# Optimization experiments

Measured on AMD Instinct MI355X. Metric: run time of the kernel, lower is better.

## Reference

```python
import jax, jax.numpy as jnp
import numpy as np

ATOM = 8          # atom_size
STRIDE = 4
NB_ATOMS = 256
LMBDA = 0.1       # l1 prox weight (prox_params)
NONDIFF = 20      # nondiff_steps (run under stop_gradient, mirroring torch.no_grad)
DIFF = 5          # diff_steps


def setup_inputs() -> dict:
    key = jax.random.key(0)
    k1, k2 = jax.random.split(key)
    y = jax.random.normal(k1, (8, 3, 256, 256), dtype=jnp.float32)
    # atoms ~ N(0,1)/sqrt(nb_channels*atom_size^2), as in __init__ with init='random'
    atoms = jax.random.normal(k2, (NB_ATOMS, 3, ATOM, ATOM), dtype=jnp.float32) / np.float32(np.sqrt(3 * ATOM * ATOM))
    return {"y": y, "atoms": atoms}


def _forward(y, atoms):
    B, C, H, W = y.shape
    a, s = ATOM, STRIDE
    Hp = (H - a) // s + 1
    Wp = (W - a) // s + 1
    D = C * a * a

    # patch row/col index grids: rows[ph, i] = ph*s + i
    rows = (jnp.arange(Hp) * s)[:, None] + jnp.arange(a)          # [Hp, a]
    cols = (jnp.arange(Wp) * s)[:, None] + jnp.arange(a)          # [Wp, a]
    R4 = rows[:, :, None, None]                                    # [Hp, a, 1, 1]
    C4 = cols[None, None, :, :]                                    # [1, 1, Wp, a]

    # unfold: extract overlapping patches -> [B, C, Hp, a, Wp, a] -> [N, D] (channel-major, matching torch)
    p6 = y[:, :, R4, C4]
    p = p6.transpose(0, 2, 4, 1, 3, 5).reshape(B * Hp * Wp, D)     # N = B*Hp*Wp

    mean = jnp.mean(p, axis=1, keepdims=True)                      # per-patch mean
    p = p - mean

    # l2-normalize atoms
    A = atoms.reshape(NB_ATOMS, D)
    A = A / jnp.linalg.norm(A, axis=1, keepdims=True)              # [nA, D]

    X = A @ A.T                                                    # [nA, nA] Gram matrix
    q = A @ p.T                                                    # [nA, N]
    L = jnp.linalg.norm(X, 2)                                      # spectral norm (Lipschitz const)
    thr = LMBDA / L

    def ista_step(c, _):
        c = c - (X @ c - q) / L
        c = jnp.sign(c) * jnp.maximum(jnp.abs(c) - thr, 0.0)       # soft-threshold prox
        return c, None

    c0 = jnp.zeros((NB_ATOMS, q.shape[1]), dtype=q.dtype)
    c, _ = jax.lax.scan(ista_step, c0, None, length=NONDIFF)
    c = jax.lax.stop_gradient(c)                                    # torch.no_grad() warmup
    c, _ = jax.lax.scan(ista_step, c, None, length=DIFF)

    # reconstruct patches: einsum('ij,il->jl') = c.T @ A, add mean back
    rec = c.T @ A + mean                                            # [N, D]
    p6r = rec.reshape(B, Hp, Wp, C, a, a).transpose(0, 3, 1, 4, 2, 5)  # [B, C, Hp, a, Wp, a]

    # fold: overlap-add patches back to image
    out = jnp.zeros((B, C, H, W), dtype=y.dtype).at[:, :, R4, C4].add(p6r)
    counts = jnp.zeros((H, W), dtype=y.dtype).at[R4, C4].add(
        jnp.ones((Hp, a, Wp, a), dtype=y.dtype))                    # overlap divisors
    return out / counts


def reference(y, atoms):
    return _forward(y, atoms)
```

## Files before the change

### kernel.cpp

```cpp
#include <hip/hip_runtime.h>
#include <math.h>

#define NPATCH 31752
#define TILE   32
#define PSTR   200
#define CSTR   264
#define MSTR   200

typedef _Float16 f16;
typedef __attribute__((ext_vector_type(2))) _Float16 f16x2;
typedef __attribute__((ext_vector_type(4))) _Float16 f16x4;
typedef __attribute__((ext_vector_type(8))) _Float16 f16x8;
typedef __attribute__((ext_vector_type(2))) __fp16   hf16x2;
typedef __attribute__((ext_vector_type(4))) float    f32x4;
#define MFMA16 __builtin_amdgcn_mfma_f32_16x16x32_f16

union HU { f16x2 h; hf16x2 g; unsigned u; };

__device__ __forceinline__ f16x2 pk2(float a, float b)
{
    HU r; r.g = __builtin_amdgcn_cvt_pkrtz(a, b);
    return r.h;
}

__device__ __forceinline__ f16x2 shrink2(f16x2 v, f16x2 thr2)
{
    HU a; a.h = v;
    unsigned sgn = a.u & 0x80008000u;
    a.u &= 0x7FFF7FFFu;
    f16x2 t = a.h - thr2;
    t = __builtin_elementwise_max(t, (f16x2)(f16)0);
    HU r; r.h = t; r.u |= sgn;
    return r.h;
}

__global__ void norm_kernel(const float* __restrict__ atoms, float* __restrict__ A,
                            float* __restrict__ As)
{
    int b = blockIdx.x, t = threadIdx.x;
    float v0 = atoms[b*192 + t];
    float v1 = atoms[b*192 + t + 64];
    float v2 = atoms[b*192 + t + 128];
    float s  = v0*v0 + v1*v1 + v2*v2;
    float r  = v0 + v1 + v2;
    #pragma unroll
    for (int m = 1; m < 64; m <<= 1) { s += __shfl_xor(s, m, 64); r += __shfl_xor(r, m, 64); }
    float rn = 1.0f / sqrtf(s);
    A[b*192 + t]       = v0 * rn;
    A[b*192 + t + 64]  = v1 * rn;
    A[b*192 + t + 128] = v2 * rn;
    if (t == 0) As[b] = r * rn;
}

__global__ void packab_kernel(const float* __restrict__ A,
                              f16* __restrict__ Ap, f16* __restrict__ Ab)
{
    int e = blockIdx.x * 256 + threadIdx.x;
    if (e < 49152) {
        int j = e & 7, lane = (e >> 3) & 63, t = e >> 9, ks = t % 6, I = t / 6;
        int row = I*16 + (lane & 15), col = ks*32 + (lane >> 4)*8 + j;
        Ap[e] = (f16)A[row*192 + col];
    } else {
        int u = e - 49152;
        int j = u & 7, lane = (u >> 3) & 63, t = u >> 9, ks = t & 7, dt = t >> 3;
        int k = ks*32 + (lane >> 4)*8 + j, d = dt*16 + (lane & 15);
        Ab[u] = (f16)A[k*192 + d];
    }
}

__global__ __launch_bounds__(256, 1)
void lchain_kernel(const f16* __restrict__ Ab, float* __restrict__ scal)
{
    __shared__ f16   mls[2 * 192 * MSTR];
    __shared__ float red[4];
    __shared__ float trc[16];
    const int tid = threadIdx.x, wv = tid >> 6, lane = tid & 63;
    const int quad = lane >> 4, l16 = lane & 15;
    const f16x8* AbV = (const f16x8*)Ab;

    f32x4 acc[3][12];
    #pragma unroll
    for (int it = 0; it < 3; ++it)
        #pragma unroll
        for (int J = 0; J < 12; ++J) acc[it][J] = (f32x4){0,0,0,0};
    for (int ks = 0; ks < 8; ++ks) {
        f16x8 bf[12];
        #pragma unroll
        for (int J = 0; J < 12; ++J) bf[J] = AbV[(J*8 + ks)*64 + lane];
        #pragma unroll
        for (int it = 0; it < 3; ++it) {
            f16x8 af = AbV[((3*wv + it)*8 + ks)*64 + lane];
            #pragma unroll
            for (int J = 0; J < 12; ++J)
                acc[it][J] = MFMA16(af, bf[J], acc[it][J], 0, 0, 0);
        }
    }
    #pragma unroll
    for (int it = 0; it < 3; ++it)
        #pragma unroll
        for (int J = 0; J < 12; ++J)
            #pragma unroll
            for (int g = 0; g < 4; ++g)
                mls[((3*wv + it)*16 + quad*4 + g)*MSTR + J*16 + l16] = (f16)acc[it][J][g];
    __syncthreads();

    float rprev = 1.0f;
    for (int t = 1; t <= 8; ++t) {
        const f16* src = mls + ((t & 1) ^ 1) * (192 * MSTR);
        f16*       dst = mls + (t & 1) * (192 * MSTR);
        const float inv = 1.0f / rprev;

        f32x4 a2[3][12];
        #pragma unroll
        for (int it = 0; it < 3; ++it)
            #pragma unroll
            for (int J = 0; J < 12; ++J) a2[it][J] = (f32x4){0,0,0,0};
        for (int ks = 0; ks < 6; ++ks) {
            f16x8 bf[12];
            #pragma unroll
            for (int J = 0; J < 12; ++J)
                bf[J] = *(const f16x8*)&src[(J*16 + l16)*MSTR + ks*32 + quad*8];
            #pragma unroll
            for (int it = 0; it < 3; ++it) {
                f16x8 af = *(const f16x8*)&src[((3*wv + it)*16 + l16)*MSTR + ks*32 + quad*8];
                #pragma unroll
                for (int J = 0; J < 12; ++J)
                    a2[it][J] = MFMA16(af, bf[J], a2[it][J], 0, 0, 0);
            }
        }
        float dsum = 0.0f;
        #pragma unroll
        for (int it = 0; it < 3; ++it) {
            int I = 3*wv + it;
            #pragma unroll
            for (int J = 0; J < 12; ++J)
                #pragma unroll
                for (int g = 0; g < 4; ++g) {
                    float v = a2[it][J][g] * inv * inv;
                    dst[(I*16 + quad*4 + g)*MSTR + J*16 + l16] = (f16)v;
                    if (J == I && l16 == quad*4 + g) dsum += v;
                }
        }
        #pragma unroll
        for (int m = 1; m < 64; m <<= 1) dsum += __shfl_xor(dsum, m, 64);
        if (lane == 0) red[wv] = dsum;
        __syncthreads();
        float r = red[0] + red[1] + red[2] + red[3];
        if (tid == 0) trc[t] = r;
        rprev = r;
        __syncthreads();
    }
    if (tid == 0) {
        float a = 0.0f;
        #pragma unroll
        for (int u = 1; u <= 8; ++u) a += exp2f(-(float)u) * log2f(trc[u]);
        float L = exp2f(a);
        scal[16] = 1.0f / L;
        scal[17] = 0.1f / L;
    }
}

__global__ void gpack_kernel(const float* __restrict__ A, const float* __restrict__ scal,
                             f16* __restrict__ Gp)
{
    __shared__ float arow[192];
    __shared__ float xrow[256];
    int i = blockIdx.x, j = threadIdx.x;
    const float invL = scal[16];
    if (j < 192) arow[j] = A[i*192 + j];
    __syncthreads();
    float s = 0.0f;
    #pragma unroll 4
    for (int d = 0; d < 192; d += 4) {
        float4 av = *(const float4*)&A[j*192 + d];
        s += arow[d]*av.x + arow[d+1]*av.y + arow[d+2]*av.z + arow[d+3]*av.w;
    }
    xrow[j] = (i == j ? 1.0f : 0.0f) - s * invL;
    __syncthreads();
    if (j < 32) {
        int ks = j >> 2, q = j & 3;
        f16x8 h;
        #pragma unroll
        for (int u = 0; u < 8; ++u) h[u] = (f16)xrow[ks*32 + q*8 + u];
        int I = i >> 4, lane = q*16 + (i & 15);
        *(f16x8*)&Gp[(((I*8 + ks)*64) + lane)*8] = h;
    }
}

__global__ __launch_bounds__(256, 2)
void mega_kernel(const float* __restrict__ y,
                 const f16* __restrict__ Gp, const f16* __restrict__ Ap,
                 const f16* __restrict__ Ab, const float* __restrict__ As,
                 const float* __restrict__ scal, float* __restrict__ out)
{
    __shared__ f16      p_lds[TILE * PSTR];
    __shared__ f16      c_lds[TILE * CSTR];
    __shared__ float    mean_lds[TILE];
    __shared__ float    msum[256];
    __shared__ unsigned pco[TILE];

    const int tid  = threadIdx.x;
    const int base = blockIdx.x * TILE;
    const int wv = tid >> 6, lane = tid & 63, quad = lane >> 4, l16 = lane & 15;
    const float invL = scal[16];
    const float thr  = scal[17];
    const f16x2 thr2 = { (f16)thr, (f16)thr };

    f16x8 greg[4][8];
    {
        const f16x8* GpV = (const f16x8*)Gp;
        #pragma unroll
        for (int rt = 0; rt < 4; ++rt)
            #pragma unroll
            for (int ks = 0; ks < 8; ++ks)
                greg[rt][ks] = GpV[((wv*4 + rt)*8 + ks)*64 + lane];
    }

    {
        int n_l = tid >> 3, qq = tid & 7;
        int n = base + n_l; if (n >= NPATCH) n = NPATCH - 1;
        int b = n / 3969, rem = n - b * 3969;
        int r = rem / 63, sc = rem - r * 63;
        if (qq == 0) pco[n_l] = ((unsigned)b << 16) | ((unsigned)r << 8) | (unsigned)sc;
        float s = 0.0f;
        #pragma unroll
        for (int u = 0; u < 3; ++u) {
            int d  = qq * 24 + u * 8;
            int ch = d >> 6, id = (d & 63) >> 3;
            const float* src = &y[((b*3 + ch)*256 + (r*4 + id))*256 + sc*4];
            float4 a = *(const float4*)src;
            float4 bq = *(const float4*)(src + 4);
            s += a.x + a.y + a.z + a.w + bq.x + bq.y + bq.z + bq.w;
            f16x8 h = { (f16)a.x, (f16)a.y, (f16)a.z, (f16)a.w,
                        (f16)bq.x, (f16)bq.y, (f16)bq.z, (f16)bq.w };
            *(f16x8*)&p_lds[n_l * PSTR + d] = h;
        }
        msum[tid] = s;
    }
    __syncthreads();
    if (tid < TILE) {
        float s = 0.0f;
        #pragma unroll
        for (int u = 0; u < 8; ++u) s += msum[tid*8 + u];
        mean_lds[tid] = s * (1.0f / 192.0f);
    }
    __syncthreads();

    f32x4 qf[4][2];
    #pragma unroll
    for (int rt = 0; rt < 4; ++rt)
        #pragma unroll
        for (int ct = 0; ct < 2; ++ct) qf[rt][ct] = (f32x4){0,0,0,0};

    const f16x8* ApV = (const f16x8*)Ap;
    #pragma unroll
    for (int ks = 0; ks < 6; ++ks) {
        f16x8 bf[2];
        #pragma unroll
        for (int ct = 0; ct < 2; ++ct)
            bf[ct] = *(const f16x8*)&p_lds[(ct*16 + l16)*PSTR + ks*32 + quad*8];
        #pragma unroll
        for (int rt = 0; rt < 4; ++rt) {
            f16x8 af = ApV[((wv*4 + rt)*6 + ks)*64 + lane];
            #pragma unroll
            for (int ct = 0; ct < 2; ++ct)
                qf[rt][ct] = MFMA16(af, bf[ct], qf[rt][ct], 0, 0, 0);
        }
    }

    f16x2 qslo[4][2], qshi[4][2];
    #pragma unroll
    for (int rt = 0; rt < 4; ++rt) {
        float a0 = As[wv*64 + rt*16 + quad*4 + 0];
        float a1 = As[wv*64 + rt*16 + quad*4 + 1];
        float a2 = As[wv*64 + rt*16 + quad*4 + 2];
        float a3 = As[wv*64 + rt*16 + quad*4 + 3];
        #pragma unroll
        for (int ct = 0; ct < 2; ++ct) {
            float mn = mean_lds[ct*16 + l16];
            float q0 = (qf[rt][ct][0] - mn*a0) * invL;
            float q1 = (qf[rt][ct][1] - mn*a1) * invL;
            float q2 = (qf[rt][ct][2] - mn*a2) * invL;
            float q3 = (qf[rt][ct][3] - mn*a3) * invL;
            f16x2 lo = pk2(q0, q1);
            f16x2 hi = pk2(q2, q3);
            qslo[rt][ct] = lo;  qshi[rt][ct] = hi;
            f16x2 clo = shrink2(lo, thr2);
            f16x2 chi = shrink2(hi, thr2);
            f16x4 cc; cc[0]=clo[0]; cc[1]=clo[1]; cc[2]=chi[0]; cc[3]=chi[1];
            *(f16x4*)&c_lds[(ct*16 + l16)*CSTR + wv*64 + rt*16 + quad*4] = cc;
        }
    }
    __syncthreads();

    for (int it = 0; it < 24; ++it) {
        f32x4 af[4][2];
        #pragma unroll
        for (int rt = 0; rt < 4; ++rt)
            #pragma unroll
            for (int ct = 0; ct < 2; ++ct) af[rt][ct] = (f32x4){0,0,0,0};

        #pragma unroll
        for (int ks = 0; ks < 8; ++ks) {
            f16x8 b0 = *(const f16x8*)&c_lds[(l16)*CSTR      + ks*32 + quad*8];
            f16x8 b1 = *(const f16x8*)&c_lds[(16 + l16)*CSTR + ks*32 + quad*8];
            #pragma unroll
            for (int rt = 0; rt < 4; ++rt) {
                af[rt][0] = MFMA16(greg[rt][ks], b0, af[rt][0], 0, 0, 0);
                af[rt][1] = MFMA16(greg[rt][ks], b1, af[rt][1], 0, 0, 0);
            }
        }
        __syncthreads();
        #pragma unroll
        for (int rt = 0; rt < 4; ++rt)
            #pragma unroll
            for (int ct = 0; ct < 2; ++ct) {
                f16x2 vlo = pk2(af[rt][ct][0], af[rt][ct][1]) + qslo[rt][ct];
                f16x2 vhi = pk2(af[rt][ct][2], af[rt][ct][3]) + qshi[rt][ct];
                vlo = shrink2(vlo, thr2);
                vhi = shrink2(vhi, thr2);
                f16x4 cc; cc[0]=vlo[0]; cc[1]=vlo[1]; cc[2]=vhi[0]; cc[3]=vhi[1];
                *(f16x4*)&c_lds[(ct*16 + l16)*CSTR + wv*64 + rt*16 + quad*4] = cc;
            }
        __syncthreads();
    }

    const int nt = wv >> 1, dtb = 6 * (wv & 1);
    f32x4 rf[6];
    #pragma unroll
    for (int u = 0; u < 6; ++u) rf[u] = (f32x4){0,0,0,0};

    const f16x8* AbV = (const f16x8*)Ab;
    #pragma unroll
    for (int ks = 0; ks < 8; ++ks) {
        f16x8 afr = *(const f16x8*)&c_lds[(nt*16 + l16)*CSTR + ks*32 + quad*8];
        #pragma unroll
        for (int u = 0; u < 6; ++u) {
            f16x8 bb = AbV[((dtb + u)*8 + ks)*64 + lane];
            rf[u] = MFMA16(afr, bb, rf[u], 0, 0, 0);
        }
    }
    #pragma unroll
    for (int g = 0; g < 4; ++g) {
        int nl = nt*16 + quad*4 + g;
        int n  = base + nl;
        if (n < NPATCH) {
            unsigned pc = pco[nl];
            int b = pc >> 16, r = (pc >> 8) & 255, sc = pc & 255;
            float mn = mean_lds[nl];
            #pragma unroll
            for (int u = 0; u < 6; ++u) {
                int d  = (dtb + u)*16 + l16;
                int ch = d >> 6, dh = (d & 63) >> 3, dw = d & 7;
                atomicAdd(&out[((b*3 + ch)*256 + (r*4 + dh))*256 + sc*4 + dw],
                          rf[u][g] + mn);
            }
        }
    }
}

__global__ void divcnt_kernel(float* __restrict__ out)
{
    int idx = blockIdx.x * 256 + threadIdx.x;
    int w = idx & 255, h = (idx >> 8) & 255;
    int rlo = max(h - 4, 0) >> 2, rhi = min(62, h >> 2);
    int slo = max(w - 4, 0) >> 2, shi = min(62, w >> 2);
    out[idx] *= 1.0f / (float)((rhi - rlo + 1) * (shi - slo + 1));
}

extern "C" void kernel_launch(void* const* d_in, const int* in_sizes, int n_in,
                              void* d_out, int out_size, void* d_ws, size_t ws_size,
                              hipStream_t stream)
{
    const float* y     = (const float*)d_in[0];
    const float* atoms = (const float*)d_in[1];
    float* out = (float*)d_out;
    float* ws  = (float*)d_ws;

    float* A    = ws;
    float* As   = ws + 49152;
    float* scal = ws + 49408;
    f16*   Ap   = (f16*)(ws + 49440);
    f16*   Ab   = (f16*)(ws + 74016);
    f16*   Gp   = (f16*)(ws + 98592);

    (void)hipMemsetAsync(d_out, 0, (size_t)out_size * sizeof(float), stream);

    norm_kernel  <<<256, 64,  0, stream>>>(atoms, A, As);
    packab_kernel<<<384, 256, 0, stream>>>(A, Ap, Ab);
    lchain_kernel<<<1, 256,   0, stream>>>(Ab, scal);
    gpack_kernel <<<256, 256, 0, stream>>>(A, scal, Gp);
    mega_kernel  <<<(NPATCH + TILE - 1) / TILE, 256, 0, stream>>>
        (y, Gp, Ap, Ab, As, scal, out);
    divcnt_kernel<<<6144, 256, 0, stream>>>(out);
}
```

Baseline: 228.7 us.

## Process two 32-patch subtiles per block with interleaved ISTA and fragment-packed LDS

Doubles the per-block tile to 64 patches, split into two 32-patch subtiles whose ISTA updates are interleaved. Each subtile's Gram-matrix MFMAs run while the other's result is written back, so there is one barrier per subtile half-step instead of a full-tile sync per iteration. The coefficient LDS buffer is rearranged into an MFMA-fragment-packed layout so B operands load as contiguous lane*8 vectors, which removes the padded stride. The cost is twice the q registers, larger LDS, and half as many blocks, which reduces grid parallelism and may lower occupancy.

```diff
diff --git a/kernel.cpp b/kernel.cpp
--- a/kernel.cpp
+++ b/kernel.cpp
@@ -2,9 +2,8 @@
 #include <math.h>
 
 #define NPATCH 31752
-#define TILE   32
+#define TILE   64
 #define PSTR   200
-#define CSTR   264
 #define MSTR   200
 
 typedef _Float16 f16;
@@ -194,9 +193,9 @@
                  const float* __restrict__ scal, float* __restrict__ out)
 {
     __shared__ f16      p_lds[TILE * PSTR];
-    __shared__ f16      c_lds[TILE * CSTR];
+    __shared__ f16      c_lds[2 * 16 * 512];
     __shared__ float    mean_lds[TILE];
-    __shared__ float    msum[256];
+    __shared__ float    msum[512];
     __shared__ unsigned pco[TILE];
 
     const int tid  = threadIdx.x;
@@ -206,6 +205,10 @@
     const float thr  = scal[17];
     const f16x2 thr2 = { (f16)thr, (f16)thr };
 
+    #define CWADDR(st, rt, ct) \
+        ((st)*8192 + ((ct)*8 + (wv*2 + ((rt)>>1)))*512 \
+         + ((((rt)&1)*2 + (quad>>1))*16 + l16)*8 + (quad&1)*4)
+
     f16x8 greg[4][8];
     {
         const f16x8* GpV = (const f16x8*)Gp;
@@ -216,8 +219,9 @@
                 greg[rt][ks] = GpV[((wv*4 + rt)*8 + ks)*64 + lane];
     }
 
-    {
-        int n_l = tid >> 3, qq = tid & 7;
+    #pragma unroll
+    for (int p = 0; p < 2; ++p) {
+        int n_l = p*32 + (tid >> 3), qq = tid & 7;
         int n = base + n_l; if (n >= NPATCH) n = NPATCH - 1;
         int b = n / 3969, rem = n - b * 3969;
         int r = rem / 63, sc = rem - r * 63;
@@ -235,60 +239,62 @@
                         (f16)bq.x, (f16)bq.y, (f16)bq.z, (f16)bq.w };
             *(f16x8*)&p_lds[n_l * PSTR + d] = h;
         }
-        msum[tid] = s;
+        msum[p*256 + tid] = s;
     }
     __syncthreads();
     if (tid < TILE) {
+        int p = tid >> 5, bse = (tid & 31) * 8;
         float s = 0.0f;
         #pragma unroll
-        for (int u = 0; u < 8; ++u) s += msum[tid*8 + u];
+        for (int u = 0; u < 8; ++u) s += msum[p*256 + bse + u];
         mean_lds[tid] = s * (1.0f / 192.0f);
     }
     __syncthreads();
 
-    f32x4 qf[4][2];
-    #pragma unroll
-    for (int rt = 0; rt < 4; ++rt)
-        #pragma unroll
-        for (int ct = 0; ct < 2; ++ct) qf[rt][ct] = (f32x4){0,0,0,0};
-
+    f16x2 qslo[2][4][2], qshi[2][4][2];
     const f16x8* ApV = (const f16x8*)Ap;
     #pragma unroll
-    for (int ks = 0; ks < 6; ++ks) {
-        f16x8 bf[2];
-        #pragma unroll
-        for (int ct = 0; ct < 2; ++ct)
-            bf[ct] = *(const f16x8*)&p_lds[(ct*16 + l16)*PSTR + ks*32 + quad*8];
+    for (int st = 0; st < 2; ++st) {
+        f32x4 qf[4][2];
+        #pragma unroll
+        for (int rt = 0; rt < 4; ++rt)
+            #pragma unroll
+            for (int ct = 0; ct < 2; ++ct) qf[rt][ct] = (f32x4){0,0,0,0};
+        #pragma unroll
+        for (int ks = 0; ks < 6; ++ks) {
+            f16x8 bf[2];
+            #pragma unroll
+            for (int ct = 0; ct < 2; ++ct)
+                bf[ct] = *(const f16x8*)&p_lds[(st*32 + ct*16 + l16)*PSTR + ks*32 + quad*8];
+            #pragma unroll
+            for (int rt = 0; rt < 4; ++rt) {
+                f16x8 af = ApV[((wv*4 + rt)*6 + ks)*64 + lane];
+                #pragma unroll
+                for (int ct = 0; ct < 2; ++ct)
+                    qf[rt][ct] = MFMA16(af, bf[ct], qf[rt][ct], 0, 0, 0);
+            }
+        }
         #pragma unroll
         for (int rt = 0; rt < 4; ++rt) {
-            f16x8 af = ApV[((wv*4 + rt)*6 + ks)*64 + lane];
-            #pragma unroll
-            for (int ct = 0; ct < 2; ++ct)
-                qf[rt][ct] = MFMA16(af, bf[ct], qf[rt][ct], 0, 0, 0);
-        }
-    }
-
-    f16x2 qslo[4][2], qshi[4][2];
-    #pragma unroll
-    for (int rt = 0; rt < 4; ++rt) {
-        float a0 = As[wv*64 + rt*16 + quad*4 + 0];
-        float a1 = As[wv*64 + rt*16 + quad*4 + 1];
-        float a2 = As[wv*64 + rt*16 + quad*4 + 2];
-        float a3 = As[wv*64 + rt*16 + quad*4 + 3];
-        #pragma unroll
-        for (int ct = 0; ct < 2; ++ct) {
-            float mn = mean_lds[ct*16 + l16];
-            float q0 = (qf[rt][ct][0] - mn*a0) * invL;
-            float q1 = (qf[rt][ct][1] - mn*a1) * invL;
-            float q2 = (qf[rt][ct][2] - mn*a2) * invL;
-            float q3 = (qf[rt][ct][3] - mn*a3) * invL;
-            f16x2 lo = pk2(q0, q1);
-            f16x2 hi = pk2(q2, q3);
-            qslo[rt][ct] = lo;  qshi[rt][ct] = hi;
-            f16x2 clo = shrink2(lo, thr2);
-            f16x2 chi = shrink2(hi, thr2);
-            f16x4 cc; cc[0]=clo[0]; cc[1]=clo[1]; cc[2]=chi[0]; cc[3]=chi[1];
-            *(f16x4*)&c_lds[(ct*16 + l16)*CSTR + wv*64 + rt*16 + quad*4] = cc;
+            float a0 = As[wv*64 + rt*16 + quad*4 + 0];
+            float a1 = As[wv*64 + rt*16 + quad*4 + 1];
+            float a2 = As[wv*64 + rt*16 + quad*4 + 2];
+            float a3 = As[wv*64 + rt*16 + quad*4 + 3];
+            #pragma unroll
+            for (int ct = 0; ct < 2; ++ct) {
+                float mn = mean_lds[st*32 + ct*16 + l16];
+                float q0 = (qf[rt][ct][0] - mn*a0) * invL;
+                float q1 = (qf[rt][ct][1] - mn*a1) * invL;
+                float q2 = (qf[rt][ct][2] - mn*a2) * invL;
+                float q3 = (qf[rt][ct][3] - mn*a3) * invL;
+                f16x2 lo = pk2(q0, q1);
+                f16x2 hi = pk2(q2, q3);
+                qslo[st][rt][ct] = lo;  qshi[st][rt][ct] = hi;
+                f16x2 clo = shrink2(lo, thr2);
+                f16x2 chi = shrink2(hi, thr2);
+                f16x4 cc; cc[0]=clo[0]; cc[1]=clo[1]; cc[2]=chi[0]; cc[3]=chi[1];
+                *(f16x4*)&c_lds[CWADDR(st, rt, ct)] = cc;
+            }
         }
     }
     __syncthreads();
@@ -299,11 +305,10 @@
         for (int rt = 0; rt < 4; ++rt)
             #pragma unroll
             for (int ct = 0; ct < 2; ++ct) af[rt][ct] = (f32x4){0,0,0,0};
-
         #pragma unroll
         for (int ks = 0; ks < 8; ++ks) {
-            f16x8 b0 = *(const f16x8*)&c_lds[(l16)*CSTR      + ks*32 + quad*8];
-            f16x8 b1 = *(const f16x8*)&c_lds[(16 + l16)*CSTR + ks*32 + quad*8];
+            f16x8 b0 = *(const f16x8*)&c_lds[(ks)*512 + lane*8];
+            f16x8 b1 = *(const f16x8*)&c_lds[(8 + ks)*512 + lane*8];
             #pragma unroll
             for (int rt = 0; rt < 4; ++rt) {
                 af[rt][0] = MFMA16(greg[rt][ks], b0, af[rt][0], 0, 0, 0);
@@ -315,48 +320,77 @@
         for (int rt = 0; rt < 4; ++rt)
             #pragma unroll
             for (int ct = 0; ct < 2; ++ct) {
-                f16x2 vlo = pk2(af[rt][ct][0], af[rt][ct][1]) + qslo[rt][ct];
-                f16x2 vhi = pk2(af[rt][ct][2], af[rt][ct][3]) + qshi[rt][ct];
+                f16x2 vlo = pk2(af[rt][ct][0], af[rt][ct][1]) + qslo[0][rt][ct];
+                f16x2 vhi = pk2(af[rt][ct][2], af[rt][ct][3]) + qshi[0][rt][ct];
                 vlo = shrink2(vlo, thr2);
                 vhi = shrink2(vhi, thr2);
                 f16x4 cc; cc[0]=vlo[0]; cc[1]=vlo[1]; cc[2]=vhi[0]; cc[3]=vhi[1];
-                *(f16x4*)&c_lds[(ct*16 + l16)*CSTR + wv*64 + rt*16 + quad*4] = cc;
-            }
+                *(f16x4*)&c_lds[CWADDR(0, rt, ct)] = cc;
+            }
+        #pragma unroll
+        for (int rt = 0; rt < 4; ++rt)
+            #pragma unroll
+            for (int ct = 0; ct < 2; ++ct) af[rt][ct] = (f32x4){0,0,0,0};
+        #pragma unroll
+        for (int ks = 0; ks < 8; ++ks) {
+            f16x8 b0 = *(const f16x8*)&c_lds[8192 + (ks)*512 + lane*8];
+            f16x8 b1 = *(const f16x8*)&c_lds[8192 + (8 + ks)*512 + lane*8];
+            #pragma unroll
+            for (int rt = 0; rt < 4; ++rt) {
+                af[rt][0] = MFMA16(greg[rt][ks], b0, af[rt][0], 0, 0, 0);
+                af[rt][1] = MFMA16(greg[rt][ks], b1, af[rt][1], 0, 0, 0);
+            }
+        }
         __syncthreads();
-    }
+        #pragma unroll
+        for (int rt = 0; rt < 4; ++rt)
+            #pragma unroll
+            for (int ct = 0; ct < 2; ++ct) {
+                f16x2 vlo = pk2(af[rt][ct][0], af[rt][ct][1]) + qslo[1][rt][ct];
+                f16x2 vhi = pk2(af[rt][ct][2], af[rt][ct][3]) + qshi[1][rt][ct];
+                vlo = shrink2(vlo, thr2);
+                vhi = shrink2(vhi, thr2);
+                f16x4 cc; cc[0]=vlo[0]; cc[1]=vlo[1]; cc[2]=vhi[0]; cc[3]=vhi[1];
+                *(f16x4*)&c_lds[CWADDR(1, rt, ct)] = cc;
+            }
+    }
+    __syncthreads();
 
     const int nt = wv >> 1, dtb = 6 * (wv & 1);
-    f32x4 rf[6];
-    #pragma unroll
-    for (int u = 0; u < 6; ++u) rf[u] = (f32x4){0,0,0,0};
-
     const f16x8* AbV = (const f16x8*)Ab;
     #pragma unroll
-    for (int ks = 0; ks < 8; ++ks) {
-        f16x8 afr = *(const f16x8*)&c_lds[(nt*16 + l16)*CSTR + ks*32 + quad*8];
-        #pragma unroll
-        for (int u = 0; u < 6; ++u) {
-            f16x8 bb = AbV[((dtb + u)*8 + ks)*64 + lane];
-            rf[u] = MFMA16(afr, bb, rf[u], 0, 0, 0);
-        }
-    }
-    #pragma unroll
-    for (int g = 0; g < 4; ++g) {
-        int nl = nt*16 + quad*4 + g;
-        int n  = base + nl;
-        if (n < NPATCH) {
-            unsigned pc = pco[nl];
-            int b = pc >> 16, r = (pc >> 8) & 255, sc = pc & 255;
-            float mn = mean_lds[nl];
+    for (int st = 0; st < 2; ++st) {
+        f32x4 rf[6];
+        #pragma unroll
+        for (int u = 0; u < 6; ++u) rf[u] = (f32x4){0,0,0,0};
+        #pragma unroll
+        for (int ks = 0; ks < 8; ++ks) {
+            f16x8 afr = *(const f16x8*)&c_lds[st*8192 + (nt*8 + ks)*512 + lane*8];
             #pragma unroll
             for (int u = 0; u < 6; ++u) {
-                int d  = (dtb + u)*16 + l16;
-                int ch = d >> 6, dh = (d & 63) >> 3, dw = d & 7;
-                atomicAdd(&out[((b*3 + ch)*256 + (r*4 + dh))*256 + sc*4 + dw],
-                          rf[u][g] + mn);
-            }
-        }
-    }
+                f16x8 bb = AbV[((dtb + u)*8 + ks)*64 + lane];
+                rf[u] = MFMA16(afr, bb, rf[u], 0, 0, 0);
+            }
+        }
+        #pragma unroll
+        for (int g = 0; g < 4; ++g) {
+            int nl = nt*16 + quad*4 + g;
+            int n  = base + st*32 + nl;
+            if (n < NPATCH) {
+                unsigned pc = pco[st*32 + nl];
+                int b = pc >> 16, r = (pc >> 8) & 255, sc = pc & 255;
+                float mn = mean_lds[st*32 + nl];
+                #pragma unroll
+                for (int u = 0; u < 6; ++u) {
+                    int d  = (dtb + u)*16 + l16;
+                    int ch = d >> 6, dh = (d & 63) >> 3, dw = d & 7;
+                    atomicAdd(&out[((b*3 + ch)*256 + (r*4 + dh))*256 + sc*4 + dw],
+                              rf[u][g] + mn);
+                }
+            }
+        }
+    }
+    #undef CWADDR
 }
 
 __global__ void divcnt_kernel(float* __restrict__ out)
```

Measured after the change: 234.6 us. +2.6%, slower.
